# Kernel tuning notes

Hardware: AMD Instinct MI355X
Metric: run time of the kernel (lower is better)

The kernel has to match this reference:

```python
import jax, jax.numpy as jnp
import numpy as np

N = 100000      # nodes on each bipartite side
E = 1600000     # edges
D_IN = 128      # input feature dim
H, C = 2, 50    # heads, per-head out channels
B = 64          # graphs in batch
NEG_SLOPE = 0.2 # GATConv leaky_relu slope


def setup_inputs() -> dict:
    key = jax.random.key(0)
    ks = jax.random.split(key, 12)
    glorot = lambda k, shape: (jax.random.uniform(k, shape, jnp.float32, -1.0, 1.0)
                               * jnp.sqrt(6.0 / (shape[0] + shape[-1])))
    return {
        "x_s": jax.random.normal(ks[0], (N, D_IN), jnp.float32),
        "x_t": jax.random.normal(ks[1], (N, D_IN), jnp.float32),
        "edge_index": jax.random.randint(ks[2], (2, E), 0, N, jnp.int64),
        "distances": jax.random.uniform(ks[3], (E,), jnp.float32),
        "x_s_batch": jnp.sort(jax.random.randint(ks[4], (N,), 0, B, jnp.int64)),
        "x_t_batch": jnp.sort(jax.random.randint(ks[5], (N,), 0, B, jnp.int64)),
        "W_src": glorot(ks[6], (D_IN, H * C)),
        "W_dst": glorot(ks[7], (D_IN, H * C)),
        "att_src": glorot(ks[8], (H, C)),
        "att_dst": glorot(ks[9], (H, C)),
        "bias_conv": jnp.zeros((H * C,), jnp.float32),
        "fc_w": glorot(ks[10], (H * C, 1)),
        "fc_b": jnp.zeros((1,), jnp.float32),
    }


def reference(x_s, x_t, edge_index, distances, x_s_batch, x_t_batch,
              W_src, W_dst, att_src, att_dst, bias_conv, fc_w, fc_b):
    src, dst = edge_index[0], edge_index[1]
    # Bipartite GATConv (edge_attr ignored: built with edge_dim=None)
    hs = (x_s @ W_src).reshape(N, H, C)            # [N,H,C]
    ht = (x_t @ W_dst).reshape(N, H, C)
    a_src = jnp.einsum('nhc,hc->nh', hs, att_src)  # [N,H]
    a_dst = jnp.einsum('nhc,hc->nh', ht, att_dst)
    e = jax.nn.leaky_relu(a_src[src] + a_dst[dst], NEG_SLOPE)   # [E,H]
    # segment softmax over edges sharing a target node
    m = jax.ops.segment_max(e, dst, num_segments=N)             # [N,H]
    ex = jnp.exp(e - m[dst])
    denom = jax.ops.segment_sum(ex, dst, num_segments=N)
    alpha = ex / (denom[dst] + 1e-16)                           # [E,H]
    # scatter-aggregate weighted source messages
    msg = alpha[:, :, None] * hs[src]                           # [E,H,C]
    out = jax.ops.segment_sum(msg, dst, num_segments=N)         # [N,H,C]
    out = out.reshape(N, H * C) + bias_conv
    x = jax.nn.relu(out)
    # global mean pool (original uses x_s_batch)
    pooled = jax.ops.segment_sum(x, x_s_batch, num_segments=B)
    counts = jax.ops.segment_sum(jnp.ones((N,), x.dtype), x_s_batch, num_segments=B)
    pooled = pooled / jnp.maximum(counts, 1.0)[:, None]         # [B,H*C]
    y = pooled @ fc_w + fc_b                                    # [B,1]
    return y.squeeze(-1)
```

## Files before the change

### kernel.cpp

```cpp
#include <hip/hip_runtime.h>
#include <math.h>

#define D_IN 128
#define HC 100
#define PW 128
#define CAP 64
#define NEG 0.2f
#define BINSH 6
#define NBIN 1563
#define BCAP 1408
#define ACH 4096
#define YSLOT 32
#define SRCM 0x1FFFF

typedef __attribute__((ext_vector_type(8))) short short8;
typedef __attribute__((ext_vector_type(4))) float f32x4;
typedef __attribute__((ext_vector_type(2))) float f32x2;

__device__ __forceinline__ float lrelu(float x){ return x > 0.f ? x : NEG*x; }

__device__ __forceinline__ unsigned short f2bf(float f){
  union { float f; unsigned u; } v; v.f = f;
  unsigned r = v.u + 0x7fffu + ((v.u >> 16) & 1u);
  return (unsigned short)(r >> 16);
}
__device__ __forceinline__ float bflo(unsigned u){
  union { unsigned x; float f; } v; v.x = u << 16; return v.f;
}
__device__ __forceinline__ float bfhi(unsigned u){
  union { unsigned x; float f; } v; v.x = u & 0xffff0000u; return v.f;
}

__global__ __launch_bounds__(256) void k_init(const float* __restrict__ Wd,
    const float* __restrict__ attd, const float* __restrict__ Ws,
    const float* __restrict__ bias, const float* __restrict__ fcw,
    const float* __restrict__ fcb, const int* __restrict__ xsb,
    float* __restrict__ wv, float* __restrict__ bias_p, float* __restrict__ fcwp,
    unsigned short* __restrict__ Wp, float* __restrict__ invb,
    int* __restrict__ bincnt, float* __restrict__ ypart,
    float* __restrict__ y, int N, int B){
  __shared__ int lo[257];
  int t = threadIdx.x;
  if (blockIdx.x == 0){
    int h = t >> 7, k = t & 127;
    float s = 0.f;
    #pragma unroll
    for (int c = 0; c < 50; ++c) s += Wd[k*HC + h*50 + c] * attd[h*50 + c];
    wv[t] = s;
    if (t < 128){
      bool cv = (t < 50) || (t >= 56 && t < 106);
      int c = (t < 50) ? t : t - 6;
      bias_p[t] = cv ? bias[c] : 0.f;
      fcwp[t]   = cv ? fcw[c]  : 0.f;
    }
    if (t < B) y[t] = fcb[0];
    for (int i = t; i < NBIN; i += 256) bincnt[i] = 0;
    if (t <= B && t < 257){
      int key = t, l = 0, hi = N;
      while (l < hi){ int mid = (l+hi)>>1; if (xsb[mid] < key) l = mid+1; else hi = mid; }
      lo[t] = l;
    }
    __syncthreads();
    if (t < B){
      int c = lo[t+1] - lo[t];
      invb[t] = 1.f / (float)((c > 0) ? c : 1);
    }
  } else if (blockIdx.x < 8){
    int ct = blockIdx.x - 1;
    int idx = ct*256 + t;
    int kk = (t >> 6) & 3, lane = t & 63;
    int kb = kk*32 + (lane >> 4)*8;
    int c  = ct*16 + (lane & 15);
    #pragma unroll
    for (int j = 0; j < 8; ++j){
      float v = (c < HC) ? Ws[(size_t)(kb + j)*HC + c] : 0.f;
      Wp[idx*8 + j] = f2bf(v);
    }
  } else {
    float4 z = make_float4(0.f,0.f,0.f,0.f);
    float4* yp4 = (float4*)ypart + (size_t)(blockIdx.x - 8)*4096;
    for (int i = t; i < 4096; i += 256) yp4[i] = z;
  }
}

__global__ __launch_bounds__(256) void k_fused(
    const float* __restrict__ x_s, const unsigned short* __restrict__ Wp,
    const float* __restrict__ atts, unsigned short* __restrict__ hsb,
    float* __restrict__ a_src,
    const float* __restrict__ x_t, const float* __restrict__ wv,
    float* __restrict__ a_dst,
    const int* __restrict__ ei, int* __restrict__ bincnt,
    int* __restrict__ ebuf,
    int N, int E, int Gb)
{
  __shared__ __align__(16) unsigned char smem[17408];
  int t = threadIdx.x;
  int bid = blockIdx.x;

  if (bid >= Gb){
    unsigned short* hls = (unsigned short*)smem;
    float* wsh = (float*)(smem + 16384);
    int lane = t & 63, w = t >> 6;
    int qr = lane & 15, qq = lane >> 4;
    int row0 = (bid - Gb)*64;

    int arow = row0 + w*16 + qr;
    bool rv = arow < N;

    const float* xtp = x_t + (size_t)arow*D_IN + qq*8;
    float4 u[8];
    #pragma unroll
    for (int kk = 0; kk < 4; ++kk){
      u[2*kk]   = rv ? *(const float4*)(xtp + kk*32)     : make_float4(0.f,0.f,0.f,0.f);
      u[2*kk+1] = rv ? *(const float4*)(xtp + kk*32 + 4) : make_float4(0.f,0.f,0.f,0.f);
    }

    wsh[t] = wv[t];
    for (int i = t; i < 4096; i += 256) ((unsigned*)hls)[i] = 0u;
    __syncthreads();

    float pd0 = 0.f, pd1 = 0.f;
    #pragma unroll
    for (int kk = 0; kk < 4; ++kk){
      float4 u0 = u[2*kk], u1 = u[2*kk+1];
      int kb = qq*8 + kk*32;
      pd0 += u0.x*wsh[kb+0] + u0.y*wsh[kb+1] + u0.z*wsh[kb+2] + u0.w*wsh[kb+3]
           + u1.x*wsh[kb+4] + u1.y*wsh[kb+5] + u1.z*wsh[kb+6] + u1.w*wsh[kb+7];
      pd1 += u0.x*wsh[128+kb+0] + u0.y*wsh[128+kb+1] + u0.z*wsh[128+kb+2] + u0.w*wsh[128+kb+3]
           + u1.x*wsh[128+kb+4] + u1.y*wsh[128+kb+5] + u1.z*wsh[128+kb+6] + u1.w*wsh[128+kb+7];
    }
    pd0 += __shfl_xor(pd0, 16, 64); pd0 += __shfl_xor(pd0, 32, 64);
    pd1 += __shfl_xor(pd1, 16, 64); pd1 += __shfl_xor(pd1, 32, 64);
    if (qq == 0 && rv){ a_dst[arow*2] = pd0; a_dst[arow*2+1] = pd1; }

    short8 afr[4];
    const float* xp = x_s + (size_t)arow*D_IN + qq*8;
    #pragma unroll
    for (int kk = 0; kk < 4; ++kk){
      float4 v0 = make_float4(0.f,0.f,0.f,0.f), v1 = v0;
      if (rv){ v0 = *(const float4*)(xp + kk*32); v1 = *(const float4*)(xp + kk*32 + 4); }
      short8 a;
      a[0]=(short)f2bf(v0.x); a[1]=(short)f2bf(v0.y); a[2]=(short)f2bf(v0.z); a[3]=(short)f2bf(v0.w);
      a[4]=(short)f2bf(v1.x); a[5]=(short)f2bf(v1.y); a[6]=(short)f2bf(v1.z); a[7]=(short)f2bf(v1.w);
      afr[kk] = a;
    }

    f32x4 acc[7];
    #pragma unroll
    for (int ct = 0; ct < 7; ++ct) acc[ct] = (f32x4){0.f,0.f,0.f,0.f};
    #pragma unroll
    for (int kk = 0; kk < 4; ++kk){
      #pragma unroll
      for (int ct = 0; ct < 7; ++ct){
        short8 b = *(const short8*)&Wp[(size_t)((ct*4+kk)*64 + lane)*8];
        acc[ct] = __builtin_amdgcn_mfma_f32_16x16x32_bf16(afr[kk], b, acc[ct], 0, 0, 0);
      }
    }

    float p0[4] = {0,0,0,0}, p1[4] = {0,0,0,0};
    #pragma unroll
    for (int ct = 0; ct < 7; ++ct){
      int c = ct*16 + qr;
      if (c < HC){
        float av = atts[c];
        #pragma unroll
        for (int r = 0; r < 4; ++r){
          float v = acc[ct][r];
          if (c < 50) p0[r] += v*av; else p1[r] += v*av;
        }
      }
    }
    #pragma unroll
    for (int d = 1; d < 16; d <<= 1){
      #pragma unroll
      for (int r = 0; r < 4; ++r){
        p0[r] += __shfl_xor(p0[r], d, 64);
        p1[r] += __shfl_xor(p1[r], d, 64);
      }
    }
    if (qr == 0){
      #pragma unroll
      for (int r = 0; r < 4; ++r){
        int row = row0 + w*16 + qq*4 + r;
        if (row < N){ a_src[row*2] = p0[r]; a_src[row*2+1] = p1[r]; }
      }
    }

    #pragma unroll
    for (int ct = 0; ct < 7; ++ct){
      int c = ct*16 + qr;
      if (c < HC){
        int p = (c < 50) ? c : c + 6;
        #pragma unroll
        for (int r = 0; r < 4; ++r)
          hls[(w*16 + qq*4 + r)*PW + p] = f2bf(acc[ct][r]);
      }
    }
    __syncthreads();
    unsigned* hg = (unsigned*)(hsb + (size_t)row0*PW);
    for (int i = t; i < 4096; i += 256) hg[i] = ((unsigned*)hls)[i];

  } else {
    int* cnt   = (int*)smem;
    int* gbase = (int*)smem + NBIN;
    int e0 = bid * ACH;
    for (int i = t; i < NBIN; i += 256) cnt[i] = 0;
    __syncthreads();

    int src[16], dst[16], rank[16];
    #pragma unroll
    for (int j = 0; j < 4; ++j){
      int e = e0 + t*16 + j*4;
      bool in = (e + 4 <= E);
      int4 s4 = in ? *(const int4*)&ei[e]     : make_int4(0,0,0,0);
      int4 d4 = in ? *(const int4*)&ei[E + e] : make_int4(-1,-1,-1,-1);
      src[j*4+0]=s4.x; src[j*4+1]=s4.y; src[j*4+2]=s4.z; src[j*4+3]=s4.w;
      dst[j*4+0]=d4.x; dst[j*4+1]=d4.y; dst[j*4+2]=d4.z; dst[j*4+3]=d4.w;
    }
    #pragma unroll
    for (int j = 0; j < 16; ++j)
      rank[j] = (dst[j] >= 0) ? atomicAdd(&cnt[dst[j] >> BINSH], 1) : -1;
    __syncthreads();
    for (int i = t; i < NBIN; i += 256)
      gbase[i] = (cnt[i] > 0) ? atomicAdd(&bincnt[i], cnt[i]) : 0;
    __syncthreads();
    #pragma unroll
    for (int j = 0; j < 16; ++j){
      if (rank[j] >= 0){
        int b = dst[j] >> BINSH;
        int gp = gbase[b] + rank[j];
        if (gp < BCAP) ebuf[(size_t)b*BCAP + gp] = src[j] | ((dst[j] & 63) << 17);
      }
    }
  }
}

__global__ __launch_bounds__(128) void k_agg(const int* __restrict__ bincnt,
    const int* __restrict__ ebuf, const float* __restrict__ a_src,
    const float* __restrict__ a_dst, const unsigned short* __restrict__ hsb,
    const float* __restrict__ bias_p, const float* __restrict__ fcwp,
    const int* __restrict__ xsb, float* __restrict__ ypart, int N)
{
  __shared__ int lsrc[32*CAP];
  __shared__ int lcnt[32];
  int t = threadIdx.x, b = blockIdx.x;
  int bin = b >> 1, half = b & 1;
  if (t < 32) lcnt[t] = 0;
  __syncthreads();
  int nE = bincnt[bin]; if (nE > BCAP) nE = BCAP;
  const int* eb = ebuf + (size_t)bin*BCAP;
  for (int i = t; i < nE; i += 128){
    int e = eb[i];
    int ld = (e >> 17) & 63;
    if ((ld >> 5) == half){
      int p = atomicAdd(&lcnt[ld & 31], 1);
      if (p < CAP) lsrc[(ld & 31)*CAP + p] = e & SRCM;
    }
  }
  __syncthreads();

  int lane = t & 63, w = t >> 6;
  int k = lane & 15, g = lane >> 4;
  bool actv = (k < 14);
  bool hsel = (k >= 7);

#define PREF(vv, e) { int s_ = __shfl(sreg, (e), 64); \
    vv = (actv && (e) < deg) ? *(const uint4*)&hsb[(size_t)s_*PW + k*8] \
                             : make_uint4(0u,0u,0u,0u); }

#define CONS(vv, e) { float a0_ = __shfl(al0, (e), 64); float a1_ = __shfl(al1, (e), 64); \
    float a_ = hsel ? a1_ : a0_; f32x2 av_ = {a_, a_}; \
    f32x2 h0_ = {bflo(vv.x), bfhi(vv.x)}; acc0 += av_*h0_; \
    f32x2 h1_ = {bflo(vv.y), bfhi(vv.y)}; acc1 += av_*h1_; \
    f32x2 h2_ = {bflo(vv.z), bfhi(vv.z)}; acc2 += av_*h2_; \
    f32x2 h3_ = {bflo(vv.w), bfhi(vv.w)}; acc3 += av_*h3_; }

  for (int it = 0; it < 16; ++it){
    int nl = w*16 + it;
    int n  = bin*64 + half*32 + nl;
    if (n >= N) break;
    int deg = lcnt[nl]; if (deg > CAP) deg = CAP;
    float2 ad = *(const float2*)&a_dst[n*2];
    int sreg = (lane < deg) ? lsrc[nl*CAP + lane] : 0;

    uint4 v0, v1, v2, v3;
    PREF(v0, g) PREF(v1, 4+g) PREF(v2, 8+g) PREF(v3, 12+g)

    float x0 = 0.f, x1 = 0.f;
    if (lane < deg){
      float2 as = *(const float2*)&a_src[sreg*2];
      x0 = __expf(fminf(lrelu(as.x + ad.x), 60.f));
      x1 = __expf(fminf(lrelu(as.y + ad.y), 60.f));
    }
    float d0 = x0, d1 = x1;
    if (deg > 32){ d0 += __shfl_xor(d0,32,64); d1 += __shfl_xor(d1,32,64); }
    if (deg > 16){ d0 += __shfl_xor(d0,16,64); d1 += __shfl_xor(d1,16,64); }
    #pragma unroll
    for (int d = 8; d >= 1; d >>= 1){ d0 += __shfl_xor(d0,d,64); d1 += __shfl_xor(d1,d,64); }
    float inv0 = __builtin_amdgcn_rcpf(d0 + 1e-16f);
    float inv1 = __builtin_amdgcn_rcpf(d1 + 1e-16f);
    float al0 = x0 * inv0, al1 = x1 * inv1;

    f32x2 acc0 = {0.f,0.f}, acc1 = {0.f,0.f}, acc2 = {0.f,0.f}, acc3 = {0.f,0.f};
    int base = 0;
    for (;;){
      CONS(v0, base+g);
      if (base + 4 >= deg) break;
      CONS(v1, base+4+g);
      if (base + 8 >= deg) break;
      CONS(v2, base+8+g);
      if (base + 12 >= deg) break;
      CONS(v3, base+12+g);
      base += 16;
      if (base >= deg) break;
      PREF(v0, base+g) PREF(v1, base+4+g) PREF(v2, base+8+g) PREF(v3, base+12+g)
    }

    float acc[8] = {acc0.x, acc0.y, acc1.x, acc1.y, acc2.x, acc2.y, acc3.x, acc3.y};
    #pragma unroll
    for (int j = 0; j < 8; ++j){
      acc[j] += __shfl_xor(acc[j], 16, 64);
      acc[j] += __shfl_xor(acc[j], 32, 64);
    }

    float s = 0.f;
    if (g == 0 && actv){
      float4 b0 = *(const float4*)&bias_p[k*8];
      float4 b1 = *(const float4*)&bias_p[k*8 + 4];
      float4 f0 = *(const float4*)&fcwp[k*8];
      float4 f1 = *(const float4*)&fcwp[k*8 + 4];
      s  = fmaxf(acc[0]+b0.x, 0.f)*f0.x + fmaxf(acc[1]+b0.y, 0.f)*f0.y
         + fmaxf(acc[2]+b0.z, 0.f)*f0.z + fmaxf(acc[3]+b0.w, 0.f)*f0.w
         + fmaxf(acc[4]+b1.x, 0.f)*f1.x + fmaxf(acc[5]+b1.y, 0.f)*f1.y
         + fmaxf(acc[6]+b1.z, 0.f)*f1.z + fmaxf(acc[7]+b1.w, 0.f)*f1.w;
    }
    #pragma unroll
    for (int d = 1; d <= 8; d <<= 1) s += __shfl_xor(s, d, 64);
    if (lane == 0){
      int bb = xsb[n];
      atomicAdd(&ypart[(size_t)((bb*YSLOT + (b & (YSLOT-1))) << 5)], s);
    }
  }
#undef PREF
#undef CONS
}

__global__ __launch_bounds__(64) void k_red(const float* __restrict__ ypart,
    const float* __restrict__ invb, float* __restrict__ y)
{
  int b = blockIdx.x, t = threadIdx.x;
  float v = (t < YSLOT) ? ypart[(size_t)((b*YSLOT + t) << 5)] : 0.f;
  #pragma unroll
  for (int d = 16; d >= 1; d >>= 1) v += __shfl_xor(v, d, 64);
  if (t == 0) y[b] += v * invb[b];
}

extern "C" void kernel_launch(void* const* d_in, const int* in_sizes, int n_in,
                              void* d_out, int out_size, void* d_ws, size_t ws_size,
                              hipStream_t stream)
{
  const float* x_s  = (const float*)d_in[0];
  const float* x_t  = (const float*)d_in[1];
  const int*   ei   = (const int*)d_in[2];
  const int*   xsb  = (const int*)d_in[4];
  const float* Ws   = (const float*)d_in[6];
  const float* Wd   = (const float*)d_in[7];
  const float* atts = (const float*)d_in[8];
  const float* attd = (const float*)d_in[9];
  const float* bias = (const float*)d_in[10];
  const float* fcw  = (const float*)d_in[11];
  const float* fcb  = (const float*)d_in[12];
  float* y = (float*)d_out;

  const int N = in_sizes[4];
  const int E = in_sizes[3];
  const int B = out_size;

  char* p = (char*)d_ws;
  auto carve = [&](size_t bytes)->char*{
    char* r = p; p += (bytes + 255) & ~(size_t)255; return r;
  };
  float*          wv     = (float*)         carve(256*4);
  float*          a_src  = (float*)         carve((size_t)N*2*4);
  float*          a_dst  = (float*)         carve((size_t)N*2*4);
  unsigned short* hsb    = (unsigned short*)carve((size_t)(N+64)*PW*2);
  float*          bias_p = (float*)         carve(128*4);
  float*          fcwp   = (float*)         carve(128*4);
  unsigned short* Wp     = (unsigned short*)carve((size_t)1792*8*2);
  float*          invb   = (float*)         carve(256*4);
  int*            bincnt = (int*)           carve(2048*4);
  float*          ypart  = (float*)         carve((size_t)B*YSLOT*32*4);
  int*            ebuf   = (int*)           carve((size_t)NBIN*BCAP*4);

  const int Gg = (N + 63) / 64;
  const int Gb = (E + ACH - 1) / ACH;

  k_init  <<<12, 256, 0, stream>>>(Wd, attd, Ws, bias, fcw, fcb, xsb,
                                   wv, bias_p, fcwp, Wp, invb, bincnt, ypart, y, N, B);
  k_fused <<<Gb + Gg, 256, 0, stream>>>(x_s, Wp, atts, hsb, a_src,
                                        x_t, wv, a_dst,
                                        ei, bincnt, ebuf, N, E, Gb);
  k_agg   <<<NBIN*2, 128, 0, stream>>>(bincnt, ebuf, a_src, a_dst, hsb,
                                       bias_p, fcwp, xsb, ypart, N);
  k_red   <<<B, 64, 0, stream>>>(ypart, invb, y);
}
```

Baseline: 262.0 us.

## Pack a_src into padding of hsb rows and compute softmax inline during aggregation

Stores the per-node source attention scores in the unused padding slots (columns 50-53) of each bf16 feature row, so the aggregation kernel reads them with the same 16-byte gather it already issues for the features. It drops the separate a_src array and its random gather. Each edge's exp weight is now computed inside the consume loop from a lane shuffle, and normalisation is deferred by scaling the accumulated sums with the reciprocal denominator at the end. This removes one dependent random load per edge and the pre-pass softmax reduction. In exchange the inner loop does extra shuffles and exps, lanes with k==6 must zero the junk channels read from the padding, and the exp is not shifted by the segment max, so it relies on the clamp at 60.

```diff
diff --git a/kernel.cpp b/kernel.cpp
--- a/kernel.cpp
+++ b/kernel.cpp
@@ -86,7 +86,6 @@
 __global__ __launch_bounds__(256) void k_fused(
     const float* __restrict__ x_s, const unsigned short* __restrict__ Wp,
     const float* __restrict__ atts, unsigned short* __restrict__ hsb,
-    float* __restrict__ a_src,
     const float* __restrict__ x_t, const float* __restrict__ wv,
     float* __restrict__ a_dst,
     const int* __restrict__ ei, int* __restrict__ bincnt,
@@ -181,8 +180,9 @@
     if (qr == 0){
       #pragma unroll
       for (int r = 0; r < 4; ++r){
-        int row = row0 + w*16 + qq*4 + r;
-        if (row < N){ a_src[row*2] = p0[r]; a_src[row*2+1] = p1[r]; }
+        int lw = w*16 + qq*4 + r;
+        *(unsigned*)&hls[lw*PW + 50] = __float_as_uint(p0[r]);
+        *(unsigned*)&hls[lw*PW + 52] = __float_as_uint(p1[r]);
       }
     }
 
@@ -236,7 +236,7 @@
 }
 
 __global__ __launch_bounds__(128) void k_agg(const int* __restrict__ bincnt,
-    const int* __restrict__ ebuf, const float* __restrict__ a_src,
+    const int* __restrict__ ebuf,
     const float* __restrict__ a_dst, const unsigned short* __restrict__ hsb,
     const float* __restrict__ bias_p, const float* __restrict__ fcwp,
     const int* __restrict__ xsb, float* __restrict__ ypart, int N)
@@ -263,13 +263,22 @@
   int k = lane & 15, g = lane >> 4;
   bool actv = (k < 14);
   bool hsel = (k >= 7);
+  int stl = (g << 4) + 6;
 
 #define PREF(vv, e) { int s_ = __shfl(sreg, (e), 64); \
     vv = (actv && (e) < deg) ? *(const uint4*)&hsb[(size_t)s_*PW + k*8] \
                              : make_uint4(0u,0u,0u,0u); }
 
-#define CONS(vv, e) { float a0_ = __shfl(al0, (e), 64); float a1_ = __shfl(al1, (e), 64); \
-    float a_ = hsel ? a1_ : a0_; f32x2 av_ = {a_, a_}; \
+#define CONS(vv, e) { \
+    unsigned ab0_ = (unsigned)__shfl((int)vv.y, stl, 64); \
+    unsigned ab1_ = (unsigned)__shfl((int)vv.z, stl, 64); \
+    float x0_ = 0.f, x1_ = 0.f; \
+    if ((e) < deg){ \
+      x0_ = __expf(fminf(lrelu(__uint_as_float(ab0_) + ad.x), 60.f)); \
+      x1_ = __expf(fminf(lrelu(__uint_as_float(ab1_) + ad.y), 60.f)); \
+    } \
+    d0 += x0_; d1 += x1_; \
+    float a_ = hsel ? x1_ : x0_; f32x2 av_ = {a_, a_}; \
     f32x2 h0_ = {bflo(vv.x), bfhi(vv.x)}; acc0 += av_*h0_; \
     f32x2 h1_ = {bflo(vv.y), bfhi(vv.y)}; acc1 += av_*h1_; \
     f32x2 h2_ = {bflo(vv.z), bfhi(vv.z)}; acc2 += av_*h2_; \
@@ -286,21 +295,7 @@
     uint4 v0, v1, v2, v3;
     PREF(v0, g) PREF(v1, 4+g) PREF(v2, 8+g) PREF(v3, 12+g)
 
-    float x0 = 0.f, x1 = 0.f;
-    if (lane < deg){
-      float2 as = *(const float2*)&a_src[sreg*2];
-      x0 = __expf(fminf(lrelu(as.x + ad.x), 60.f));
-      x1 = __expf(fminf(lrelu(as.y + ad.y), 60.f));
-    }
-    float d0 = x0, d1 = x1;
-    if (deg > 32){ d0 += __shfl_xor(d0,32,64); d1 += __shfl_xor(d1,32,64); }
-    if (deg > 16){ d0 += __shfl_xor(d0,16,64); d1 += __shfl_xor(d1,16,64); }
-    #pragma unroll
-    for (int d = 8; d >= 1; d >>= 1){ d0 += __shfl_xor(d0,d,64); d1 += __shfl_xor(d1,d,64); }
-    float inv0 = __builtin_amdgcn_rcpf(d0 + 1e-16f);
-    float inv1 = __builtin_amdgcn_rcpf(d1 + 1e-16f);
-    float al0 = x0 * inv0, al1 = x1 * inv1;
-
+    float d0 = 0.f, d1 = 0.f;
     f32x2 acc0 = {0.f,0.f}, acc1 = {0.f,0.f}, acc2 = {0.f,0.f}, acc3 = {0.f,0.f};
     int base = 0;
     for (;;){
@@ -316,6 +311,12 @@
       PREF(v0, base+g) PREF(v1, base+4+g) PREF(v2, base+8+g) PREF(v3, base+12+g)
     }
 
+    d0 += __shfl_xor(d0, 16, 64); d0 += __shfl_xor(d0, 32, 64);
+    d1 += __shfl_xor(d1, 16, 64); d1 += __shfl_xor(d1, 32, 64);
+    float inv0 = __builtin_amdgcn_rcpf(d0 + 1e-16f);
+    float inv1 = __builtin_amdgcn_rcpf(d1 + 1e-16f);
+    float sc = hsel ? inv1 : inv0;
+
     float acc[8] = {acc0.x, acc0.y, acc1.x, acc1.y, acc2.x, acc2.y, acc3.x, acc3.y};
     #pragma unroll
     for (int j = 0; j < 8; ++j){
@@ -325,14 +326,18 @@
 
     float s = 0.f;
     if (g == 0 && actv){
+      if (k == 6){
+        acc[2] = 0.f; acc[3] = 0.f; acc[4] = 0.f;
+        acc[5] = 0.f; acc[6] = 0.f; acc[7] = 0.f;
+      }
       float4 b0 = *(const float4*)&bias_p[k*8];
       float4 b1 = *(const float4*)&bias_p[k*8 + 4];
       float4 f0 = *(const float4*)&fcwp[k*8];
       float4 f1 = *(const float4*)&fcwp[k*8 + 4];
-      s  = fmaxf(acc[0]+b0.x, 0.f)*f0.x + fmaxf(acc[1]+b0.y, 0.f)*f0.y
-         + fmaxf(acc[2]+b0.z, 0.f)*f0.z + fmaxf(acc[3]+b0.w, 0.f)*f0.w
-         + fmaxf(acc[4]+b1.x, 0.f)*f1.x + fmaxf(acc[5]+b1.y, 0.f)*f1.y
-         + fmaxf(acc[6]+b1.z, 0.f)*f1.z + fmaxf(acc[7]+b1.w, 0.f)*f1.w;
+      s  = fmaxf(acc[0]*sc+b0.x, 0.f)*f0.x + fmaxf(acc[1]*sc+b0.y, 0.f)*f0.y
+         + fmaxf(acc[2]*sc+b0.z, 0.f)*f0.z + fmaxf(acc[3]*sc+b0.w, 0.f)*f0.w
+         + fmaxf(acc[4]*sc+b1.x, 0.f)*f1.x + fmaxf(acc[5]*sc+b1.y, 0.f)*f1.y
+         + fmaxf(acc[6]*sc+b1.z, 0.f)*f1.z + fmaxf(acc[7]*sc+b1.w, 0.f)*f1.w;
     }
     #pragma unroll
     for (int d = 1; d <= 8; d <<= 1) s += __shfl_xor(s, d, 64);
@@ -381,7 +386,6 @@
     char* r = p; p += (bytes + 255) & ~(size_t)255; return r;
   };
   float*          wv     = (float*)         carve(256*4);
-  float*          a_src  = (float*)         carve((size_t)N*2*4);
   float*          a_dst  = (float*)         carve((size_t)N*2*4);
   unsigned short* hsb    = (unsigned short*)carve((size_t)(N+64)*PW*2);
   float*          bias_p = (float*)         carve(128*4);
@@ -397,10 +401,10 @@
 
   k_init  <<<12, 256, 0, stream>>>(Wd, attd, Ws, bias, fcw, fcb, xsb,
                                    wv, bias_p, fcwp, Wp, invb, bincnt, ypart, y, N, B);
-  k_fused <<<Gb + Gg, 256, 0, stream>>>(x_s, Wp, atts, hsb, a_src,
+  k_fused <<<Gb + Gg, 256, 0, stream>>>(x_s, Wp, atts, hsb,
                                         x_t, wv, a_dst,
                                         ei, bincnt, ebuf, N, E, Gb);
-  k_agg   <<<NBIN*2, 128, 0, stream>>>(bincnt, ebuf, a_src, a_dst, hsb,
+  k_agg   <<<NBIN*2, 128, 0, stream>>>(bincnt, ebuf, a_dst, hsb,
                                        bias_p, fcwp, xsb, ypart, N);
   k_red   <<<B, 64, 0, stream>>>(ypart, invb, y);
 }
```

Result: no change. 265.6 us (+1.4%).
